# Kernel optimization log

Measured on AMD Instinct MI355X. Metric: run time of the kernel, lower is better.

## Reference

```python
import jax, jax.numpy as jnp
import numpy as np

N, IN_CAPS, OUT_CAPS, IN_LEN, OUT_LEN = 64, 256, 128, 16, 32
NUM_ITERATIONS = 3


def _squash(t, axis=-1):
    # scale * t / sqrt(||t||^2) with scale = ||t||^2 / (1 + ||t||^2)
    sq = jnp.sum(t * t, axis=axis, keepdims=True)
    return (sq / (1.0 + sq)) * t / jnp.sqrt(sq)


def setup_inputs() -> dict:
    key = jax.random.key(0)
    k1, k2 = jax.random.split(key)
    x = jax.random.normal(k1, (N, IN_CAPS, IN_LEN), dtype=jnp.float32)
    weight = jax.random.normal(k2, (OUT_CAPS, IN_CAPS, IN_LEN, OUT_LEN), dtype=jnp.float32)
    return {"x": x, "weight": weight}


def reference(x, weight):
    # priors: [out_caps, N, in_caps, out_len]  (torch keeps an extra singleton dim)
    priors = jnp.einsum('nik,oikl->onil', x, weight)
    logits = jnp.zeros_like(priors)
    outputs = None
    for i in range(NUM_ITERATIONS):
        # torch softmax(dim=2) == softmax over the in_caps axis
        probs = jax.nn.softmax(logits, axis=2)
        s = jnp.sum(probs * priors, axis=2, keepdims=True)  # [O, N, 1, L]
        outputs = _squash(s, axis=-1)
        if i != NUM_ITERATIONS - 1:
            # delta broadcasts over out_len, as in the torch code
            logits = logits + jnp.sum(priors * outputs, axis=-1, keepdims=True)
    # squeeze routing dim, transpose to [N, out_caps, out_len]
    return jnp.transpose(outputs[:, :, 0, :], (1, 0, 2))
```

## Files before the change

### kernel.cpp

```cpp
#include <hip/hip_runtime.h>


#define ICAPS 256
#define OCAPS 128
#define WS_WC 0ull
#define WS_XC 67108864ull
#define WS_NEED 68157440ull

typedef __attribute__((ext_vector_type(8))) short s16x8;
typedef __attribute__((ext_vector_type(16))) float f32x16;

__device__ inline unsigned bfbits(float f) {
    unsigned u = __float_as_uint(f);
    return (u + 0x7FFFu + ((u >> 16) & 1u)) & 0xFFFF0000u;
}

__global__ __launch_bounds__(512)
void caps_prep(const float* __restrict__ x, const float* __restrict__ w,
               unsigned char* __restrict__ ws) {
    const int wv = threadIdx.x >> 6, lane = threadIdx.x & 63;
    uint4* WC = (uint4*)(ws + WS_WC);
    uint4* XC = (uint4*)(ws + WS_XC);
    const int gid = blockIdx.x * 8 + wv;

    float f[8];
    if (gid < 32768) {
        const int l = lane & 31, kb = (lane >> 5) * 8;
        const float* src = w + ((size_t)gid * 16 + kb) * 32 + l;
        #pragma unroll
        for (int j = 0; j < 8; ++j) f[j] = src[j * 32];
        unsigned h[4], g[4];
        #pragma unroll
        for (int c = 0; c < 4; ++c) {
            unsigned b0 = bfbits(f[2 * c]), b1 = bfbits(f[2 * c + 1]);
            h[c] = (b0 >> 16) | (b1 & 0xFFFF0000u);
            float l0 = f[2 * c] - __uint_as_float(b0);
            float l1 = f[2 * c + 1] - __uint_as_float(b1);
            g[c] = (bfbits(l0) >> 16) | (bfbits(l1) & 0xFFFF0000u);
        }
        const size_t idx = ((size_t)gid * 64 + lane) * 2;
        WC[idx]     = make_uint4(h[0], h[1], h[2], h[3]);
        WC[idx + 1] = make_uint4(g[0], g[1], g[2], g[3]);
    } else {
        const int id = gid - 32768;
        const int nh = id >> 8, i = id & 255;
        const int np = lane & 31, kb = (lane >> 5) * 8;
        const float* src = x + ((size_t)(nh * 32 + np) * ICAPS + i) * 16 + kb;
        const float4 a = *(const float4*)src;
        const float4 b = *(const float4*)(src + 4);
        f[0] = a.x; f[1] = a.y; f[2] = a.z; f[3] = a.w;
        f[4] = b.x; f[5] = b.y; f[6] = b.z; f[7] = b.w;
        unsigned h[4], g[4];
        #pragma unroll
        for (int c = 0; c < 4; ++c) {
            unsigned b0 = bfbits(f[2 * c]), b1 = bfbits(f[2 * c + 1]);
            h[c] = (b0 >> 16) | (b1 & 0xFFFF0000u);
            float l0 = f[2 * c] - __uint_as_float(b0);
            float l1 = f[2 * c + 1] - __uint_as_float(b1);
            g[c] = (bfbits(l0) >> 16) | (bfbits(l1) & 0xFFFF0000u);
        }
        const size_t idx = ((size_t)id * 64 + lane) * 2;
        XC[idx]     = make_uint4(h[0], h[1], h[2], h[3]);
        XC[idx + 1] = make_uint4(g[0], g[1], g[2], g[3]);
    }
}

__global__ __launch_bounds__(512)
void caps_main(const unsigned char* __restrict__ ws, float* __restrict__ out) {
    __shared__ float lg[ICAPS * 32];
    __shared__ float slab[8 * 1280];
    __shared__ float svv[32 * 33];
    __shared__ float zz[8 * 32];
    __shared__ float zinv[32];

    const int t = threadIdx.x, wv = t >> 6, lane = t & 63;
    const int o = blockIdx.x & 127, nh = blockIdx.x >> 7;
    const int n = lane & 31, half = lane >> 5;

    const s16x8* Wp = (const s16x8*)(ws + WS_WC) + ((size_t)o * ICAPS * 64 + lane) * 2;
    const s16x8* Xp = (const s16x8*)(ws + WS_XC) + ((size_t)nh * ICAPS * 64 + lane) * 2;

    float vr[16];
    const int ibase = wv * 32;

    for (int pass = 0; pass < 3; ++pass) {
        float uacc[16];
        #pragma unroll
        for (int r = 0; r < 16; ++r) uacc[r] = 0.f;
        float z = 0.f;

        s16x8 C[8], Nx[8];
        {
            const size_t b0 = (size_t)ibase * 128;
            C[0] = Wp[b0];       C[1] = Wp[b0 + 1];
            C[2] = Xp[b0];       C[3] = Xp[b0 + 1];
            C[4] = Wp[b0 + 128]; C[5] = Wp[b0 + 129];
            C[6] = Xp[b0 + 128]; C[7] = Xp[b0 + 129];
        }

        if (pass == 0) {
            f32x16 Pa = {}, Pb = {};
            for (int bb = 0; bb < 16; ++bb) {
                if (bb < 15) {
                    const size_t bn = (size_t)(ibase + 2 * (bb + 1)) * 128;
                    Nx[0] = Wp[bn];       Nx[1] = Wp[bn + 1];
                    Nx[2] = Xp[bn];       Nx[3] = Xp[bn + 1];
                    Nx[4] = Wp[bn + 128]; Nx[5] = Wp[bn + 129];
                    Nx[6] = Xp[bn + 128]; Nx[7] = Xp[bn + 129];
                }
                Pa = __builtin_amdgcn_mfma_f32_32x32x16_bf16(C[1], C[2], Pa, 0, 0, 0);
                Pb = __builtin_amdgcn_mfma_f32_32x32x16_bf16(C[5], C[6], Pb, 0, 0, 0);
                Pa = __builtin_amdgcn_mfma_f32_32x32x16_bf16(C[0], C[3], Pa, 0, 0, 0);
                Pb = __builtin_amdgcn_mfma_f32_32x32x16_bf16(C[4], C[7], Pb, 0, 0, 0);
                Pa = __builtin_amdgcn_mfma_f32_32x32x16_bf16(C[0], C[2], Pa, 0, 0, 0);
                Pb = __builtin_amdgcn_mfma_f32_32x32x16_bf16(C[4], C[6], Pb, 0, 0, 0);
                if (bb < 15) {
                    #pragma unroll
                    for (int j = 0; j < 8; ++j) C[j] = Nx[j];
                }
            }
            #pragma unroll
            for (int r = 0; r < 16; ++r) uacc[r] = Pa[r] + Pb[r];
        } else {
            for (int bb = 0; bb < 16; ++bb) {
                if (bb < 15) {
                    const size_t bn = (size_t)(ibase + 2 * (bb + 1)) * 128;
                    Nx[0] = Wp[bn];       Nx[1] = Wp[bn + 1];
                    Nx[2] = Xp[bn];       Nx[3] = Xp[bn + 1];
                    Nx[4] = Wp[bn + 128]; Nx[5] = Wp[bn + 129];
                    Nx[6] = Xp[bn + 128]; Nx[7] = Xp[bn + 129];
                }
                f32x16 P0 = {}, P1 = {};
                P0 = __builtin_amdgcn_mfma_f32_32x32x16_bf16(C[1], C[2], P0, 0, 0, 0);
                P1 = __builtin_amdgcn_mfma_f32_32x32x16_bf16(C[5], C[6], P1, 0, 0, 0);
                P0 = __builtin_amdgcn_mfma_f32_32x32x16_bf16(C[0], C[3], P0, 0, 0, 0);
                P1 = __builtin_amdgcn_mfma_f32_32x32x16_bf16(C[4], C[7], P1, 0, 0, 0);
                P0 = __builtin_amdgcn_mfma_f32_32x32x16_bf16(C[0], C[2], P0, 0, 0, 0);
                P1 = __builtin_amdgcn_mfma_f32_32x32x16_bf16(C[4], C[6], P1, 0, 0, 0);

                #pragma unroll
                for (int j = 0; j < 2; ++j) {
                    const f32x16& P = j ? P1 : P0;
                    const int i = ibase + bb * 2 + j;
                    float da = P[0] * vr[0];
                    float db = P[8] * vr[8];
                    #pragma unroll
                    for (int r = 1; r < 8; ++r) {
                        da = fmaf(P[r], vr[r], da);
                        db = fmaf(P[r + 8], vr[r + 8], db);
                    }
                    float d = da + db;
                    d += __shfl_xor(d, 32);
                    if (pass == 1) {
                        if (half == 0) lg[i * 32 + n] = d;
                    } else {
                        d += lg[i * 32 + n];
                    }
                    const float e = __expf(d);
                    z += e;
                    #pragma unroll
                    for (int r = 0; r < 16; ++r) uacc[r] = fmaf(e, P[r], uacc[r]);
                }
                if (bb < 15) {
                    #pragma unroll
                    for (int j = 0; j < 8; ++j) C[j] = Nx[j];
                }
            }
        }

        #pragma unroll
        for (int c = 0; c < 4; ++c)
            *(float4*)(&slab[wv * 1280 + lane * 20 + c * 4]) =
                make_float4(uacc[4 * c], uacc[4 * c + 1], uacc[4 * c + 2], uacc[4 * c + 3]);
        if (pass > 0 && half == 0) zz[wv * 32 + n] = z;
        __syncthreads();

        #pragma unroll
        for (int hh = 0; hh < 2; ++hh) {
            const int e = t + hh * 512;
            const int lw = e >> 4, r = e & 15;
            float s = 0.f;
            #pragma unroll
            for (int w8 = 0; w8 < 8; ++w8) s += slab[w8 * 1280 + lw * 20 + r];
            const int nn = lw & 31, ll = (r & 3) + 8 * (r >> 2) + 4 * (lw >> 5);
            svv[nn * 33 + ll] = s;
        }
        if (t < 32) {
            if (pass == 0) zinv[t] = 1.0f / 256.0f;
            else {
                float zs = 0.f;
                #pragma unroll
                for (int w8 = 0; w8 < 8; ++w8) zs += zz[w8 * 32 + t];
                zinv[t] = 1.0f / zs;
            }
        }
        __syncthreads();

        {
            const int nq = t >> 4, sub = t & 15;
            const float a = svv[nq * 33 + sub] * zinv[nq];
            const float b = svv[nq * 33 + sub + 16] * zinv[nq];
            float sq = a * a + b * b;
            #pragma unroll
            for (int m = 1; m < 16; m <<= 1) sq += __shfl_xor(sq, m, 16);
            const float sc = sqrtf(sq) / (1.0f + sq);
            if (pass == 2) {
                const int ng = nh * 32 + nq;
                out[((size_t)ng * OCAPS + o) * 32 + sub] = a * sc;
                out[((size_t)ng * OCAPS + o) * 32 + sub + 16] = b * sc;
            } else {
                svv[nq * 33 + sub] = a * sc;
                svv[nq * 33 + sub + 16] = b * sc;
            }
        }
        if (pass < 2) {
            __syncthreads();
            #pragma unroll
            for (int r = 0; r < 16; ++r) {
                const int l = (r & 3) + 8 * (r >> 2) + 4 * half;
                vr[r] = svv[n * 33 + l];
            }
        }
    }
}

#define KLEN  16
#define LLEN  32
#define TN    16
#define LGS   257
#define XROW  20
#define XIST  (TN * XROW + 4)
#define SVS   33
#define RBS   33
#define NSTG  32
#define NSTEP (ICAPS / NSTG)

__global__ __launch_bounds__(512, 2)
void caps_route_fb(const float* __restrict__ xg_all,
                   const float* __restrict__ wg_all,
                   float* __restrict__ out) {
    __shared__ float lg[TN * LGS];
    __shared__ float xt[NSTG * XIST];
    __shared__ float sv[TN * SVS];
    __shared__ float zz[8][TN];
    __shared__ float zinv[TN];

    const int t   = threadIdx.x;
    const int o   = blockIdx.x & 127;
    const int n0  = (blockIdx.x >> 7) * TN;
    const int isp = t >> 4;
    const int lb  = (t >> 2) & 3;
    const int nb  = t & 3;
    const int l0  = lb * 8;

    const float* xg = xg_all + (size_t)n0 * ICAPS * KLEN;
    const float* wg = wg_all + (size_t)o * ICAPS * KLEN * LLEN;

    for (int pass = 0; pass < 3; ++pass) {
        float u[4][8];
        float zq[4] = {0.f, 0.f, 0.f, 0.f};
        #pragma unroll
        for (int q = 0; q < 4; ++q)
            #pragma unroll
            for (int r = 0; r < 8; ++r) u[q][r] = 0.f;

        for (int st = 0; st < NSTEP; ++st) {
            const int i0 = st * NSTG;
            __syncthreads();
            #pragma unroll
            for (int j = 0; j < 4; ++j) {
                const int g   = j * 512 + t;
                const int nn  = g >> 7;
                const int rem = g & 127;
                const int il  = rem >> 2;
                const int k4c = rem & 3;
                *(float4*)(&xt[il * XIST + nn * XROW + k4c * 4]) =
                    *(const float4*)(xg + (size_t)(nn * ICAPS + i0 + il) * KLEN + k4c * 4);
            }
            __syncthreads();

            const int i = i0 + isp;
            const float* wp = wg + (size_t)i * (KLEN * LLEN) + l0;
            const float* xp = &xt[isp * XIST];
            float P[4][8];
            #pragma unroll
            for (int q = 0; q < 4; ++q)
                #pragma unroll
                for (int r = 0; r < 8; ++r) P[q][r] = 0.f;

            #pragma unroll
            for (int k4 = 0; k4 < 4; ++k4) {
                float xq[4][4];
                #pragma unroll
                for (int q = 0; q < 4; ++q)
                    *(float4*)(&xq[q][0]) = *(const float4*)(xp + (nb + 4 * q) * XROW + k4 * 4);
                #pragma unroll
                for (int kk = 0; kk < 4; ++kk) {
                    const int k = k4 * 4 + kk;
                    const float4 wa = *(const float4*)(wp + k * LLEN);
                    const float4 wb = *(const float4*)(wp + k * LLEN + 4);
                    #pragma unroll
                    for (int q = 0; q < 4; ++q) {
                        const float xv = xq[q][kk];
                        P[q][0] = fmaf(xv, wa.x, P[q][0]);
                        P[q][1] = fmaf(xv, wa.y, P[q][1]);
                        P[q][2] = fmaf(xv, wa.z, P[q][2]);
                        P[q][3] = fmaf(xv, wa.w, P[q][3]);
                        P[q][4] = fmaf(xv, wb.x, P[q][4]);
                        P[q][5] = fmaf(xv, wb.y, P[q][5]);
                        P[q][6] = fmaf(xv, wb.z, P[q][6]);
                        P[q][7] = fmaf(xv, wb.w, P[q][7]);
                    }
                }
            }

            if (pass == 0) {
                #pragma unroll
                for (int q = 0; q < 4; ++q)
                    #pragma unroll
                    for (int r = 0; r < 8; ++r) u[q][r] += P[q][r];
            } else {
                #pragma unroll
                for (int q = 0; q < 4; ++q) {
                    const float* vp = &sv[(nb + 4 * q) * SVS + l0];
                    float d = P[q][0] * vp[0] + P[q][1] * vp[1] + P[q][2] * vp[2] + P[q][3] * vp[3]
                            + P[q][4] * vp[4] + P[q][5] * vp[5] + P[q][6] * vp[6] + P[q][7] * vp[7];
                    d += __shfl_xor(d, 4);
                    d += __shfl_xor(d, 8);
                    float lnew = d;
                    if (pass == 2) lnew += lg[(nb + 4 * q) * LGS + i];
                    else if (lb == 0) lg[(nb + 4 * q) * LGS + i] = lnew;
                    const float e = __expf(lnew);
                    zq[q] += e;
                    #pragma unroll
                    for (int r = 0; r < 8; ++r) u[q][r] = fmaf(e, P[q][r], u[q][r]);
                }
            }
        }

        #pragma unroll
        for (int q = 0; q < 4; ++q) {
            #pragma unroll
            for (int r = 0; r < 8; ++r) {
                float v = u[q][r];
                v += __shfl_xor(v, 16);
                v += __shfl_xor(v, 32);
                u[q][r] = v;
            }
            float zv = zq[q];
            zv += __shfl_xor(zv, 16);
            zv += __shfl_xor(zv, 32);
            zq[q] = zv;
        }
        __syncthreads();
        {
            const int wvv = t >> 6, lane = t & 63;
            if (lane < 16) {
                float* rb = &xt[wvv * (16 * RBS) + lane * RBS];
                #pragma unroll
                for (int q = 0; q < 4; ++q)
                    #pragma unroll
                    for (int r = 0; r < 8; ++r) rb[q * 8 + r] = u[q][r];
            }
            if (pass > 0 && lane < 4) {
                #pragma unroll
                for (int q = 0; q < 4; ++q) zz[wvv][lane + 4 * q] = zq[q];
            }
        }
        __syncthreads();
        {
            const int low4 = t >> 5, qr = t & 31;
            const int qq = qr >> 3, rr = qr & 7;
            const int lbb = low4 >> 2, nbb = low4 & 3;
            float ssum = 0.f;
            #pragma unroll
            for (int w8 = 0; w8 < 8; ++w8) ssum += xt[w8 * (16 * RBS) + low4 * RBS + qr];
            sv[(nbb + 4 * qq) * SVS + lbb * 8 + rr] = ssum;
        }
        if (t < TN) {
            if (pass == 0) zinv[t] = 1.0f / 256.0f;
            else {
                float zs = 0.f;
                #pragma unroll
                for (int w8 = 0; w8 < 8; ++w8) zs += zz[w8][t];
                zinv[t] = 1.0f / zs;
            }
        }
        __syncthreads();
        {
            const int nn = t >> 5, l = t & 31;
            const float val = sv[nn * SVS + l] * zinv[nn];
            float sq = val * val;
            #pragma unroll
            for (int m = 1; m < 32; m <<= 1) sq += __shfl_xor(sq, m, 32);
            const float sc = sqrtf(sq) / (1.0f + sq);
            if (pass == 2)
                out[((size_t)(n0 + nn) * OCAPS + o) * LLEN + l] = val * sc;
            else
                sv[nn * SVS + l] = val * sc;
        }
    }
}

extern "C" void kernel_launch(void* const* d_in, const int* in_sizes, int n_in,
                              void* d_out, int out_size, void* d_ws, size_t ws_size,
                              hipStream_t stream) {
    const float* x = (const float*)d_in[0];
    const float* w = (const float*)d_in[1];
    float* outp = (float*)d_out;
    if (ws_size >= WS_NEED) {
        caps_prep<<<dim3(4160), dim3(512), 0, stream>>>(x, w, (unsigned char*)d_ws);
        caps_main<<<dim3(256), dim3(512), 0, stream>>>((const unsigned char*)d_ws, outp);
    } else {
        caps_route_fb<<<dim3(512), dim3(512), 0, stream>>>(x, w, outp);
    }
}
```

Measured before the change: 151.5 us.

## Coalesce weight prep via LDS transpose and split hi/lo into separate planes

The prep kernel now reads weights with contiguous float4 loads and transposes them through a padded shared-memory tile, replacing the strided 32-float-apart scalar loads. The hi and lo bf16 parts are written as separate 64-lane planes instead of interleaved pairs, so stores and main-kernel loads are contiguous per plane. bf16 packing now uses a byte-permute instruction. This adds a block barrier and LDS traffic in prep, and the main kernel's load indexing changes to match the new layout.

Result: faster. 143.6 us (-5.3%).

```diff
diff --git a/kernel.cpp b/kernel.cpp
--- a/kernel.cpp
+++ b/kernel.cpp
@@ -3,65 +3,81 @@
 
 #define ICAPS 256
 #define OCAPS 128
-#define WS_WC 0ull
 #define WS_XC 67108864ull
 #define WS_NEED 68157440ull
+#define KPAD 20
 
 typedef __attribute__((ext_vector_type(8))) short s16x8;
 typedef __attribute__((ext_vector_type(16))) float f32x16;
 
-__device__ inline unsigned bfbits(float f) {
-    unsigned u = __float_as_uint(f);
-    return (u + 0x7FFFu + ((u >> 16) & 1u)) & 0xFFFF0000u;
+union u4s8 { unsigned u[4]; s16x8 v; };
+
+__device__ inline unsigned rne_adj(unsigned u) {
+    return u + 0x7FFFu + ((u >> 16) & 1u);
+}
+
+__device__ inline void split8(const float* f, s16x8& hi, s16x8& lo) {
+    u4s8 H, L;
+    #pragma unroll
+    for (int c = 0; c < 4; ++c) {
+        const unsigned u0 = __float_as_uint(f[2 * c]);
+        const unsigned u1 = __float_as_uint(f[2 * c + 1]);
+        const unsigned r0 = rne_adj(u0), r1 = rne_adj(u1);
+        H.u[c] = __builtin_amdgcn_perm(r1, r0, 0x07060302u);
+        const float h0 = __uint_as_float(r0 & 0xFFFF0000u);
+        const float h1 = __uint_as_float(r1 & 0xFFFF0000u);
+        const unsigned l0 = rne_adj(__float_as_uint(f[2 * c] - h0));
+        const unsigned l1 = rne_adj(__float_as_uint(f[2 * c + 1] - h1));
+        L.u[c] = __builtin_amdgcn_perm(l1, l0, 0x07060302u);
+    }
+    hi = H.v; lo = L.v;
 }
 
 __global__ __launch_bounds__(512)
 void caps_prep(const float* __restrict__ x, const float* __restrict__ w,
                unsigned char* __restrict__ ws) {
+    __shared__ float T[8][32 * KPAD];
     const int wv = threadIdx.x >> 6, lane = threadIdx.x & 63;
-    uint4* WC = (uint4*)(ws + WS_WC);
-    uint4* XC = (uint4*)(ws + WS_XC);
     const int gid = blockIdx.x * 8 + wv;
-
     float f[8];
+    s16x8 hi, lo;
+
     if (gid < 32768) {
-        const int l = lane & 31, kb = (lane >> 5) * 8;
-        const float* src = w + ((size_t)gid * 16 + kb) * 32 + l;
-        #pragma unroll
-        for (int j = 0; j < 8; ++j) f[j] = src[j * 32];
-        unsigned h[4], g[4];
-        #pragma unroll
-        for (int c = 0; c < 4; ++c) {
-            unsigned b0 = bfbits(f[2 * c]), b1 = bfbits(f[2 * c + 1]);
-            h[c] = (b0 >> 16) | (b1 & 0xFFFF0000u);
-            float l0 = f[2 * c] - __uint_as_float(b0);
-            float l1 = f[2 * c + 1] - __uint_as_float(b1);
-            g[c] = (bfbits(l0) >> 16) | (bfbits(l1) & 0xFFFF0000u);
-        }
-        const size_t idx = ((size_t)gid * 64 + lane) * 2;
-        WC[idx]     = make_uint4(h[0], h[1], h[2], h[3]);
-        WC[idx + 1] = make_uint4(g[0], g[1], g[2], g[3]);
-    } else {
+        const float* src = w + (size_t)gid * 512 + lane * 8;
+        const float4 a = *(const float4*)src;
+        const float4 b = *(const float4*)(src + 4);
+        const float v[8] = {a.x, a.y, a.z, a.w, b.x, b.y, b.z, b.w};
+        {
+            float* Tw = &T[wv][0];
+            const int k = lane >> 2, l0 = (lane & 3) * 8;
+            #pragma unroll
+            for (int j = 0; j < 8; ++j) Tw[(l0 + j) * KPAD + k] = v[j];
+        }
+        __syncthreads();
+        {
+            const float* rd = &T[wv][(lane & 31) * KPAD + (lane >> 5) * 8];
+            const float4 ra = *(const float4*)rd;
+            const float4 rb = *(const float4*)(rd + 4);
+            f[0] = ra.x; f[1] = ra.y; f[2] = ra.z; f[3] = ra.w;
+            f[4] = rb.x; f[5] = rb.y; f[6] = rb.z; f[7] = rb.w;
+        }
+        split8(f, hi, lo);
+        s16x8* WC = (s16x8*)ws;
+        WC[(size_t)gid * 128 + lane] = hi;
+        WC[(size_t)gid * 128 + 64 + lane] = lo;
+    } else if (gid < 33280) {
         const int id = gid - 32768;
         const int nh = id >> 8, i = id & 255;
-        const int np = lane & 31, kb = (lane >> 5) * 8;
-        const float* src = x + ((size_t)(nh * 32 + np) * ICAPS + i) * 16 + kb;
+        const int n = lane & 31, kb = (lane >> 5) * 8;
+        const float* src = x + ((size_t)(nh * 32 + n) * ICAPS + i) * 16 + kb;
         const float4 a = *(const float4*)src;
         const float4 b = *(const float4*)(src + 4);
         f[0] = a.x; f[1] = a.y; f[2] = a.z; f[3] = a.w;
         f[4] = b.x; f[5] = b.y; f[6] = b.z; f[7] = b.w;
-        unsigned h[4], g[4];
-        #pragma unroll
-        for (int c = 0; c < 4; ++c) {
-            unsigned b0 = bfbits(f[2 * c]), b1 = bfbits(f[2 * c + 1]);
-            h[c] = (b0 >> 16) | (b1 & 0xFFFF0000u);
-            float l0 = f[2 * c] - __uint_as_float(b0);
-            float l1 = f[2 * c + 1] - __uint_as_float(b1);
-            g[c] = (bfbits(l0) >> 16) | (bfbits(l1) & 0xFFFF0000u);
-        }
-        const size_t idx = ((size_t)id * 64 + lane) * 2;
-        XC[idx]     = make_uint4(h[0], h[1], h[2], h[3]);
-        XC[idx + 1] = make_uint4(g[0], g[1], g[2], g[3]);
+        split8(f, hi, lo);
+        s16x8* XC = (s16x8*)(ws + WS_XC);
+        XC[(size_t)id * 128 + lane] = hi;
+        XC[(size_t)id * 128 + 64 + lane] = lo;
     }
 }
 
@@ -77,8 +93,8 @@
     const int o = blockIdx.x & 127, nh = blockIdx.x >> 7;
     const int n = lane & 31, half = lane >> 5;
 
-    const s16x8* Wp = (const s16x8*)(ws + WS_WC) + ((size_t)o * ICAPS * 64 + lane) * 2;
-    const s16x8* Xp = (const s16x8*)(ws + WS_XC) + ((size_t)nh * ICAPS * 64 + lane) * 2;
+    const s16x8* Wp = (const s16x8*)ws + (size_t)o * ICAPS * 128 + lane;
+    const s16x8* Xp = (const s16x8*)(ws + WS_XC) + (size_t)nh * ICAPS * 128 + lane;
 
     float vr[16];
     const int ibase = wv * 32;
@@ -92,10 +108,10 @@
         s16x8 C[8], Nx[8];
         {
             const size_t b0 = (size_t)ibase * 128;
-            C[0] = Wp[b0];       C[1] = Wp[b0 + 1];
-            C[2] = Xp[b0];       C[3] = Xp[b0 + 1];
-            C[4] = Wp[b0 + 128]; C[5] = Wp[b0 + 129];
-            C[6] = Xp[b0 + 128]; C[7] = Xp[b0 + 129];
+            C[0] = Wp[b0];       C[1] = Wp[b0 + 64];
+            C[2] = Xp[b0];       C[3] = Xp[b0 + 64];
+            C[4] = Wp[b0 + 128]; C[5] = Wp[b0 + 192];
+            C[6] = Xp[b0 + 128]; C[7] = Xp[b0 + 192];
         }
 
         if (pass == 0) {
@@ -103,10 +119,10 @@
             for (int bb = 0; bb < 16; ++bb) {
                 if (bb < 15) {
                     const size_t bn = (size_t)(ibase + 2 * (bb + 1)) * 128;
-                    Nx[0] = Wp[bn];       Nx[1] = Wp[bn + 1];
-                    Nx[2] = Xp[bn];       Nx[3] = Xp[bn + 1];
-                    Nx[4] = Wp[bn + 128]; Nx[5] = Wp[bn + 129];
-                    Nx[6] = Xp[bn + 128]; Nx[7] = Xp[bn + 129];
+                    Nx[0] = Wp[bn];       Nx[1] = Wp[bn + 64];
+                    Nx[2] = Xp[bn];       Nx[3] = Xp[bn + 64];
+                    Nx[4] = Wp[bn + 128]; Nx[5] = Wp[bn + 192];
+                    Nx[6] = Xp[bn + 128]; Nx[7] = Xp[bn + 192];
                 }
                 Pa = __builtin_amdgcn_mfma_f32_32x32x16_bf16(C[1], C[2], Pa, 0, 0, 0);
                 Pb = __builtin_amdgcn_mfma_f32_32x32x16_bf16(C[5], C[6], Pb, 0, 0, 0);
@@ -125,10 +141,10 @@
             for (int bb = 0; bb < 16; ++bb) {
                 if (bb < 15) {
                     const size_t bn = (size_t)(ibase + 2 * (bb + 1)) * 128;
-                    Nx[0] = Wp[bn];       Nx[1] = Wp[bn + 1];
-                    Nx[2] = Xp[bn];       Nx[3] = Xp[bn + 1];
-                    Nx[4] = Wp[bn + 128]; Nx[5] = Wp[bn + 129];
-                    Nx[6] = Xp[bn + 128]; Nx[7] = Xp[bn + 129];
+                    Nx[0] = Wp[bn];       Nx[1] = Wp[bn + 64];
+                    Nx[2] = Xp[bn];       Nx[3] = Xp[bn + 64];
+                    Nx[4] = Wp[bn + 128]; Nx[5] = Wp[bn + 192];
+                    Nx[6] = Xp[bn + 128]; Nx[7] = Xp[bn + 192];
                 }
                 f32x16 P0 = {}, P1 = {};
                 P0 = __builtin_amdgcn_mfma_f32_32x32x16_bf16(C[1], C[2], P0, 0, 0, 0);
```
